# Kernel tuning notes

Measured on AMD Instinct MI355X. Metric: run time of the kernel, lower is better.

The kernel has to match this reference:

```python
import jax, jax.numpy as jnp
import numpy as np
import math

N_HEADS = 8
LN_EPS = 1e-5

def _layernorm(x, g, b):
    m = jnp.mean(x, axis=-1, keepdims=True)
    v = jnp.var(x, axis=-1, keepdims=True)
    return (x - m) / jnp.sqrt(v + LN_EPS) * g + b

def _elu_feature(x):
    return jax.nn.elu(x) + 1.0

def _recurrence(Q, K, V, decay, reverse):
    # Q,K,V: (B,H,T,d); decay: (H,)
    B, H, T, d = Q.shape
    lamS = decay[None, :, None, None]
    lamz = decay[None, :, None]
    def step(carry, inp):
        S, z = carry
        q, k, v = inp
        S = lamS * S + k[..., :, None] * v[..., None, :]       # (B,H,d,d)
        z = lamz * z + k                                        # (B,H,d)
        y_raw = jnp.einsum('bhd,bhde->bhe', q, S)
        c_raw = jnp.sum(q * z, axis=-1)
        qk = jnp.sum(q * k, axis=-1, keepdims=True)
        return (S, z), (y_raw - 0.5 * qk * v, c_raw - 0.5 * qk[..., 0])
    S0 = jnp.zeros((B, H, d, d), Q.dtype)
    z0 = jnp.zeros((B, H, d), Q.dtype)
    qs = jnp.moveaxis(Q, 2, 0)
    ks = jnp.moveaxis(K, 2, 0)
    vs = jnp.moveaxis(V, 2, 0)
    _, (Y, C) = jax.lax.scan(step, (S0, z0), (qs, ks, vs), reverse=reverse)
    return jnp.moveaxis(Y, 0, 2), jnp.moveaxis(C, 0, 2)  # (B,H,T,d),(B,H,T)

def setup_inputs() -> dict:
    B, T, D, F = 2, 2048, 512, 2048
    key = jax.random.key(0)
    ks = jax.random.split(key, 8)
    std = 0.02
    return {
        'x': jax.random.normal(ks[0], (B, T, D), jnp.float32),
        'mask': jnp.zeros((B, T), dtype=bool),
        'Wq': jax.random.normal(ks[1], (D, D), jnp.float32) * std,
        'Wk': jax.random.normal(ks[2], (D, D), jnp.float32) * std,
        'Wv': jax.random.normal(ks[3], (D, D), jnp.float32) * std,
        'Wo': jax.random.normal(ks[4], (D, D), jnp.float32) * std,
        'bo': jnp.zeros((D,), jnp.float32),
        'g1': jnp.ones((D,), jnp.float32),
        'b1': jnp.zeros((D,), jnp.float32),
        'g2': jnp.ones((D,), jnp.float32),
        'b2': jnp.zeros((D,), jnp.float32),
        'W1': jax.random.normal(ks[5], (F, D), jnp.float32) * std,
        'bf1': jnp.zeros((F,), jnp.float32),
        'W2': jax.random.normal(ks[6], (D, F), jnp.float32) * std,
        'bf2': jnp.zeros((D,), jnp.float32),
        'decay_logit': jnp.full((N_HEADS,), math.log(9.0), jnp.float32),
    }

def reference(x, mask, Wq, Wk, Wv, Wo, bo, g1, b1, g2, b2, W1, bf1, W2, bf2, decay_logit):
    B, T, D = x.shape
    H = N_HEADS
    hd = D // H
    residual = x
    xn = _layernorm(x, g1, b1)
    def proj(W):
        return jnp.einsum('btd,od->bto', xn, W).reshape(B, T, H, hd).transpose(0, 2, 1, 3)
    Q = _elu_feature(proj(Wq))
    K = _elu_feature(proj(Wk))
    V = proj(Wv)
    pad = (~mask).astype(x.dtype)[:, None, :, None]  # (B,1,T,1)
    K = K * pad
    V = V * pad
    decay = jax.nn.sigmoid(decay_logit)
    Yf, Cf = _recurrence(Q, K, V, decay, reverse=False)
    Yb, Cb = _recurrence(Q, K, V, decay, reverse=True)
    denom = jnp.clip((Cf + Cb)[..., None], 1e-6)
    out = (Yf + Yb) / denom                       # (B,H,T,d)
    out = out.transpose(0, 2, 1, 3).reshape(B, T, D)
    out = jnp.einsum('btd,od->bto', out, Wo) + bo
    x = residual + out
    h = _layernorm(x, g2, b2)
    ffn = jnp.einsum('btd,fd->btf', h, W1) + bf1
    ffn = jax.nn.gelu(ffn, approximate=False)
    ffn = jnp.einsum('btf,df->btd', ffn, W2) + bf2
    return x + ffn
```

## Files before the change

### kernel.cpp

```cpp
#include <hip/hip_runtime.h>
#include <math.h>

#define BB 2
#define TT 2048
#define DD 512
#define FF 2048
#define HH 8
#define BT 4096
#define NC 32
#define CK 64

typedef __bf16 bf16_t;
typedef bf16_t bf16x8 __attribute__((ext_vector_type(8)));
typedef bf16_t bf16x4 __attribute__((ext_vector_type(4)));
typedef float f32x4 __attribute__((ext_vector_type(4)));

typedef const __attribute__((address_space(1))) void* gas_p;
typedef __attribute__((address_space(3))) void* las_p;

__device__ __forceinline__ void async16(const void* g, void* l) {
  __builtin_amdgcn_global_load_lds((gas_p)g, (las_p)l, 16, 0, 0);
}

#define PIPE_SYNC(vm) asm volatile("s_waitcnt lgkmcnt(0) vmcnt(" vm ")\n\ts_barrier" ::: "memory")

__global__ __launch_bounds__(256) void ln_cast_kernel(
    const float* __restrict__ x, const float* __restrict__ g, const float* __restrict__ bb,
    bf16_t* __restrict__ out,
    const float* __restrict__ Wq, const float* __restrict__ Wk,
    const float* __restrict__ Wv, const float* __restrict__ Wo,
    const float* __restrict__ W1, const float* __restrict__ W2,
    bf16_t* __restrict__ wdst) {
  int t = threadIdx.x;
  if (blockIdx.x >= BT) {
    size_t i = ((size_t)(blockIdx.x - BT) * 256 + t) * 8;
    const float* src; size_t off;
    if (i < 262144)       { src = Wq; off = i; }
    else if (i < 524288)  { src = Wk; off = i - 262144; }
    else if (i < 786432)  { src = Wv; off = i - 524288; }
    else if (i < 1048576) { src = Wo; off = i - 786432; }
    else if (i < 2097152) { src = W1; off = i - 1048576; }
    else                  { src = W2; off = i - 2097152; }
    float4 a = *(const float4*)(src + off);
    float4 b = *(const float4*)(src + off + 4);
    bf16x8 o;
    o[0] = (bf16_t)a.x; o[1] = (bf16_t)a.y; o[2] = (bf16_t)a.z; o[3] = (bf16_t)a.w;
    o[4] = (bf16_t)b.x; o[5] = (bf16_t)b.y; o[6] = (bf16_t)b.z; o[7] = (bf16_t)b.w;
    *(bf16x8*)(wdst + i) = o;
    return;
  }
  int row = blockIdx.x;
  const float* xr = x + (size_t)row * DD;
  float v0 = xr[t], v1 = xr[t + 256];
  float s = v0 + v1, sq = v0 * v0 + v1 * v1;
  for (int o = 32; o; o >>= 1) { s += __shfl_down(s, o); sq += __shfl_down(sq, o); }
  __shared__ float red[8];
  __shared__ float mv[2];
  int w = t >> 6;
  if ((t & 63) == 0) { red[w] = s; red[4 + w] = sq; }
  __syncthreads();
  if (t == 0) {
    float S = red[0] + red[1] + red[2] + red[3];
    float Q = red[4] + red[5] + red[6] + red[7];
    float m = S * (1.f / 512.f);
    float var = Q * (1.f / 512.f) - m * m;
    mv[0] = m; mv[1] = rsqrtf(var + 1e-5f);
  }
  __syncthreads();
  float m = mv[0], r = mv[1];
  out[(size_t)row * DD + t]       = (bf16_t)((v0 - m) * r * g[t] + bb[t]);
  out[(size_t)row * DD + t + 256] = (bf16_t)((v1 - m) * r * g[t + 256] + bb[t + 256]);
}

template<int MODE>
__global__ __launch_bounds__(256) void mfma_gemm(
    const bf16_t* __restrict__ A, const bf16_t* __restrict__ B, int K, int NT,
    bf16_t* __restrict__ Qo, bf16_t* __restrict__ Ko, bf16_t* __restrict__ Vo,
    bf16_t* __restrict__ Ob, const float* __restrict__ bias,
    const unsigned char* __restrict__ mask) {
  __shared__ __align__(16) bf16_t smem[3 * 8192];
  int tid = threadIdx.x;
  int bid = blockIdx.x;
  int xcd = bid & 7;
  int tmp = bid >> 3;
  int nt = tmp % NT;
  int mt = (tmp / NT) * 8 + xcd;
  int n0 = nt * 128, m0 = mt * 128;
  int elt = tid * 8;
  int srow = elt >> 5, scol = elt & 31;
  const bf16_t* Ag = A + (size_t)(m0 + srow) * K + scol;
  const bf16_t* Bg = B + (size_t)(n0 + srow) * K + scol;
  size_t hstep = (size_t)64 * K;
  int NS = K >> 5;
#define ISSUE(s) { bf16_t* st = smem + ((s) % 3) * 8192; int k0 = (s) * 32; \
    async16(Ag + k0, st + elt); async16(Ag + k0 + hstep, st + 2048 + elt); \
    async16(Bg + k0, st + 4096 + elt); async16(Bg + k0 + hstep, st + 6144 + elt); }
  ISSUE(0); ISSUE(1);
  f32x4 acc[4][4] = {};
  int w = tid >> 6, l = tid & 63;
  int wm = (w >> 1) * 64, wn = (w & 1) * 64;
  int fr = l & 15, fk = (l >> 4) * 8;
  for (int i = 0; i < NS; i++) {
    if (i < NS - 1) PIPE_SYNC("4");
    else            PIPE_SYNC("0");
    if (i + 2 < NS) ISSUE(i + 2);
    const bf16_t* As = smem + (i % 3) * 8192;
    const bf16_t* Bs = As + 4096;
    bf16x8 af[4], bfr[4];
#pragma unroll
    for (int ii = 0; ii < 4; ii++) af[ii] = *(const bf16x8*)&As[(wm + ii * 16 + fr) * 32 + fk];
#pragma unroll
    for (int j = 0; j < 4; j++) bfr[j] = *(const bf16x8*)&Bs[(wn + j * 16 + fr) * 32 + fk];
#pragma unroll
    for (int ii = 0; ii < 4; ii++)
#pragma unroll
      for (int j = 0; j < 4; j++)
        acc[ii][j] = __builtin_amdgcn_mfma_f32_16x16x32_bf16(af[ii], bfr[j], acc[ii][j], 0, 0, 0);
  }
#undef ISSUE
  __syncthreads();
  const int CST = 136;
  int cn = l & 15, cr = (l >> 4) * 4;
  bf16_t* outp;
  int ldc, ncol0;
  if (MODE == 0) {
    int seg = n0 >> 9;
    outp = seg == 0 ? Qo : (seg == 1 ? Ko : Vo);
    ldc = 512; ncol0 = n0 & 511;
  } else {
    outp = Ob; ldc = 2048; ncol0 = n0;
  }
#pragma unroll
  for (int i = 0; i < 4; i++) {
#pragma unroll
    for (int r = 0; r < 4; r++) {
      int mrow = wm + i * 16 + cr + r;
      float p = 1.f;
      if (MODE == 0) p = mask[m0 + mrow] ? 0.f : 1.f;
#pragma unroll
      for (int j = 0; j < 4; j++) {
        int ncol = wn + j * 16 + cn;
        float v = acc[i][j][r];
        float ov;
        if (MODE == 0) {
          int seg = n0 >> 9;
          float e = v > 0.f ? v + 1.f : expf(v);
          ov = seg == 0 ? e : (seg == 1 ? e * p : v * p);
        } else {
          float t2 = v + bias[ncol0 + ncol];
          ov = 0.5f * t2 * (1.f + erff(t2 * 0.70710678118654752f));
        }
        smem[mrow * CST + ncol] = (bf16_t)ov;
      }
    }
  }
  __syncthreads();
#pragma unroll
  for (int it = 0; it < 8; it++) {
    int vec = tid + it * 256;
    int row = vec >> 4;
    int col = (vec & 15) * 8;
    bf16x8 v8 = *(const bf16x8*)&smem[row * CST + col];
    *(bf16x8*)(outp + (size_t)(m0 + row) * ldc + ncol0 + col) = v8;
  }
}

template<int KPER>
__global__ __launch_bounds__(256) void mfma_gemm_pk(
    const bf16_t* __restrict__ A, const bf16_t* __restrict__ B, int Kst,
    bf16_t* __restrict__ P0, bf16_t* __restrict__ P1) {
  __shared__ __align__(16) bf16_t smem[4 * 6144];
  int tid = threadIdx.x;
  int bid = blockIdx.x;
  int xcd = bid & 7;
  int tmp = bid >> 3;
  int nt = tmp & 7;
  int mt = (tmp >> 3) * 8 + xcd;
  int n0 = nt * 64, m0 = mt * 128;
  int kb = blockIdx.y * KPER;
  bf16_t* P = blockIdx.y ? P1 : P0;
  int elt = tid * 8;
  int arow = elt >> 5, acol = elt & 31;
  const bf16_t* Ag = A + (size_t)(m0 + arow) * Kst + acol;
  const bf16_t* Bg = B + (size_t)(n0 + arow) * Kst + acol;
  size_t hstep = (size_t)64 * Kst;
  const int NS = KPER >> 5;
#define ISSUE(s) { bf16_t* st = smem + ((s) & 3) * 6144; int k0 = kb + (s) * 32; \
    async16(Ag + k0, st + elt); async16(Ag + k0 + hstep, st + 2048 + elt); \
    async16(Bg + k0, st + 4096 + elt); }
  ISSUE(0); ISSUE(1); ISSUE(2);
  f32x4 acc[4][2] = {};
  int w = tid >> 6, l = tid & 63;
  int wm = (w >> 1) * 64, wn = (w & 1) * 32;
  int fr = l & 15, fk = (l >> 4) * 8;
  for (int i = 0; i < NS; i++) {
    int rem = NS - 1 - i;
    if (rem >= 2)      PIPE_SYNC("6");
    else if (rem == 1) PIPE_SYNC("3");
    else               PIPE_SYNC("0");
    if (i + 3 < NS) ISSUE(i + 3);
    const bf16_t* As = smem + (i & 3) * 6144;
    const bf16_t* Bs = As + 4096;
    bf16x8 af[4], bfr[2];
#pragma unroll
    for (int ii = 0; ii < 4; ii++) af[ii] = *(const bf16x8*)&As[(wm + ii * 16 + fr) * 32 + fk];
#pragma unroll
    for (int j = 0; j < 2; j++) bfr[j] = *(const bf16x8*)&Bs[(wn + j * 16 + fr) * 32 + fk];
#pragma unroll
    for (int ii = 0; ii < 4; ii++)
#pragma unroll
      for (int j = 0; j < 2; j++)
        acc[ii][j] = __builtin_amdgcn_mfma_f32_16x16x32_bf16(af[ii], bfr[j], acc[ii][j], 0, 0, 0);
  }
#undef ISSUE
  __syncthreads();
  const int PST = 72;
  int cn = l & 15, cr = (l >> 4) * 4;
#pragma unroll
  for (int i = 0; i < 4; i++)
#pragma unroll
    for (int r = 0; r < 4; r++) {
      int mrow = wm + i * 16 + cr + r;
#pragma unroll
      for (int j = 0; j < 2; j++) {
        int ncol = wn + j * 16 + cn;
        smem[mrow * PST + ncol] = (bf16_t)acc[i][j][r];
      }
    }
  __syncthreads();
#pragma unroll
  for (int it = 0; it < 4; it++) {
    int vec = tid + it * 256;
    int row = vec >> 3;
    int col = (vec & 7) * 8;
    bf16x8 v8 = *(const bf16x8*)&smem[row * PST + col];
    *(bf16x8*)(P + (size_t)(m0 + row) * 512 + n0 + col) = v8;
  }
}

__global__ __launch_bounds__(256) void reduce2_kernel(
    const bf16_t* __restrict__ P0, const bf16_t* __restrict__ P1,
    const float* __restrict__ bias, const float* __restrict__ resid,
    float* __restrict__ o) {
  size_t idx = ((size_t)blockIdx.x * 256 + threadIdx.x) * 4;
  int n = (int)(idx & 511);
  bf16x4 a4 = *(const bf16x4*)(P0 + idx);
  bf16x4 b4 = *(const bf16x4*)(P1 + idx);
  float4 rr = *(const float4*)(resid + idx);
  float4 bi = *(const float4*)(bias + n);
  *(float4*)(o + idx) = make_float4(
      (float)a4[0] + (float)b4[0] + bi.x + rr.x,
      (float)a4[1] + (float)b4[1] + bi.y + rr.y,
      (float)a4[2] + (float)b4[2] + bi.z + rr.z,
      (float)a4[3] + (float)b4[3] + bi.w + rr.w);
}

__global__ __launch_bounds__(256) void reduce_ln_kernel(
    const bf16_t* __restrict__ P0, const bf16_t* __restrict__ P1,
    const float* __restrict__ bias, const float* __restrict__ resid,
    float* __restrict__ x2, const float* __restrict__ g, const float* __restrict__ bb,
    bf16_t* __restrict__ out) {
  int row = blockIdx.x;
  int t = threadIdx.x;
  size_t o0 = (size_t)row * DD + t;
  size_t o1 = o0 + 256;
  float v0 = (float)P0[o0] + (float)P1[o0] + bias[t] + resid[o0];
  float v1 = (float)P0[o1] + (float)P1[o1] + bias[t + 256] + resid[o1];
  x2[o0] = v0; x2[o1] = v1;
  float s = v0 + v1, sq = v0 * v0 + v1 * v1;
  for (int o = 32; o; o >>= 1) { s += __shfl_down(s, o); sq += __shfl_down(sq, o); }
  __shared__ float red[8];
  __shared__ float mv[2];
  int w = t >> 6;
  if ((t & 63) == 0) { red[w] = s; red[4 + w] = sq; }
  __syncthreads();
  if (t == 0) {
    float S = red[0] + red[1] + red[2] + red[3];
    float Q = red[4] + red[5] + red[6] + red[7];
    float m = S * (1.f / 512.f);
    float var = Q * (1.f / 512.f) - m * m;
    mv[0] = m; mv[1] = rsqrtf(var + 1e-5f);
  }
  __syncthreads();
  float m = mv[0], r = mv[1];
  out[o0] = (bf16_t)((v0 - m) * r * g[t] + bb[t]);
  out[o1] = (bf16_t)((v1 - m) * r * g[t + 256] + bb[t + 256]);
}

__global__ __launch_bounds__(256) void chunk_summary_kernel(
    const bf16_t* __restrict__ Kb, const bf16_t* __restrict__ Vb,
    const float* __restrict__ dl, bf16_t* __restrict__ Sst, float* __restrict__ zst) {
  int chunk = blockIdx.x, bh = blockIdx.y;
  int b = bh >> 3, h = bh & 7;
  int t0 = chunk * CK;
  int tid = threadIdx.x;
  __shared__ __align__(16) float Ks[64][64];
  __shared__ __align__(16) float Vs[64][64];
  __shared__ float pw[72];
  float lam = 1.f / (1.f + expf(-dl[h]));
  if (tid <= 64) pw[tid] = powf(lam, (float)tid);
  int lrow = tid >> 2, lq = tid & 3;
  for (int q = 0; q < 2; q++) {
    int c = lq * 16 + q * 8;
    size_t g = ((size_t)(b * TT + t0 + lrow)) * DD + (size_t)h * 64 + c;
    bf16x8 k8 = *(const bf16x8*)(Kb + g);
    bf16x8 v8 = *(const bf16x8*)(Vb + g);
#pragma unroll
    for (int u = 0; u < 8; u++) { Ks[lrow][c + u] = (float)k8[u]; Vs[lrow][c + u] = (float)v8[u]; }
  }
  __syncthreads();
  int e1 = tid & 63;
  int e2b = (tid >> 6) * 16;
  float af_[16], ab_[16];
#pragma unroll
  for (int r = 0; r < 16; r++) { af_[r] = 0.f; ab_[r] = 0.f; }
  float zf = 0.f, zb = 0.f;
  for (int j = 0; j < 64; j++) {
    float kj = Ks[j][e1];
    float kf = pw[63 - j] * kj;
    float kb2 = pw[j] * kj;
    if (tid < 64) { zf += kf; zb += kb2; }
#pragma unroll
    for (int rr = 0; rr < 16; rr += 4) {
      float4 v4 = *(const float4*)&Vs[j][e2b + rr];
      af_[rr]     += kf * v4.x;  ab_[rr]     += kb2 * v4.x;
      af_[rr + 1] += kf * v4.y;  ab_[rr + 1] += kb2 * v4.y;
      af_[rr + 2] += kf * v4.z;  ab_[rr + 2] += kb2 * v4.z;
      af_[rr + 3] += kf * v4.w;  ab_[rr + 3] += kb2 * v4.w;
    }
  }
  size_t bfr = ((size_t)bh * NC + chunk) * 4096;
  size_t bbr = (((size_t)16 + bh) * NC + chunk) * 4096;
#pragma unroll
  for (int r = 0; r < 16; r++) {
    Sst[bfr + (size_t)(e2b + r) * 64 + e1] = (bf16_t)af_[r];
    Sst[bbr + (size_t)(e2b + r) * 64 + e1] = (bf16_t)ab_[r];
  }
  if (tid < 64) {
    zst[((size_t)bh * NC + chunk) * 64 + tid] = zf;
    zst[(((size_t)16 + bh) * NC + chunk) * 64 + tid] = zb;
  }
}

__global__ __launch_bounds__(1024) void scan_kernel(bf16_t* __restrict__ Sst,
                                                    float* __restrict__ zst,
                                                    const float* __restrict__ dl) {
  int bh = blockIdx.x, dir = blockIdx.y;
  int h = bh & 7;
  int tid = threadIdx.x;
  float lam = 1.f / (1.f + expf(-dl[h]));
  float lamC = powf(lam, 64.f);
  size_t base = ((size_t)dir * 16 + bh) * (size_t)NC * 4096 + (size_t)tid * 4;
  float s0 = 0.f, s1 = 0.f, s2 = 0.f, s3 = 0.f;
  for (int g = 0; g < 4; g++) {
    bf16x4 L[8];
#pragma unroll
    for (int i = 0; i < 8; i++) {
      int s = g * 8 + i;
      int c = dir ? (NC - 1 - s) : s;
      L[i] = *(bf16x4*)(Sst + base + (size_t)c * 4096);
    }
#pragma unroll
    for (int i = 0; i < 8; i++) {
      int s = g * 8 + i;
      int c = dir ? (NC - 1 - s) : s;
      s0 = s0 * lamC + (float)L[i][0];
      s1 = s1 * lamC + (float)L[i][1];
      s2 = s2 * lamC + (float)L[i][2];
      s3 = s3 * lamC + (float)L[i][3];
      bf16x4 o;
      o[0] = (bf16_t)s0; o[1] = (bf16_t)s1; o[2] = (bf16_t)s2; o[3] = (bf16_t)s3;
      *(bf16x4*)(Sst + base + (size_t)c * 4096) = o;
    }
  }
  if (tid < 64) {
    size_t zb = ((size_t)dir * 16 + bh) * (size_t)NC * 64 + tid;
    float z = 0.f;
    for (int g = 0; g < 4; g++) {
      float zL[8];
#pragma unroll
      for (int i = 0; i < 8; i++) {
        int s = g * 8 + i;
        int c = dir ? (NC - 1 - s) : s;
        zL[i] = zst[zb + (size_t)c * 64];
      }
#pragma unroll
      for (int i = 0; i < 8; i++) {
        int s = g * 8 + i;
        int c = dir ? (NC - 1 - s) : s;
        z = z * lamC + zL[i];
        zst[zb + (size_t)c * 64] = z;
      }
    }
  }
}

#define AST 72
__global__ __launch_bounds__(256) void chunk_attn_kernel(
    const bf16_t* __restrict__ Qb, const bf16_t* __restrict__ Kb, const bf16_t* __restrict__ Vb,
    const bf16_t* __restrict__ Sst, const float* __restrict__ zst, const float* __restrict__ dl,
    bf16_t* __restrict__ attnb) {
  int chunk = blockIdx.x, bh = blockIdx.y;
  int b = bh >> 3, h = bh & 7;
  int t0 = chunk * CK;
  int tid = threadIdx.x;
  __shared__ __align__(16) bf16_t Qa[64 * AST];
  __shared__ __align__(16) bf16_t KA[64 * AST];
  __shared__ __align__(16) bf16_t Vt[64 * AST];
  __shared__ __align__(16) bf16_t Sft[64 * AST];
  __shared__ __align__(16) bf16_t Sbt[64 * AST];
  __shared__ float rowpart[64][16];
  __shared__ float zpf[64], zpb[64];
  __shared__ float den[64];
  __shared__ float pw[72];
  float lam = 1.f / (1.f + expf(-dl[h]));
  if (tid <= 64) pw[tid] = powf(lam, (float)tid);
  int lrow = tid >> 2, lq = tid & 3;
  for (int q = 0; q < 2; q++) {
    int c = lq * 16 + q * 8;
    size_t g = ((size_t)(b * TT + t0 + lrow)) * DD + (size_t)h * 64 + c;
    bf16x8 q8 = *(const bf16x8*)(Qb + g);
    bf16x8 k8 = *(const bf16x8*)(Kb + g);
    bf16x8 v8 = *(const bf16x8*)(Vb + g);
    *(bf16x8*)&Qa[lrow * AST + c] = q8;
    *(bf16x8*)&KA[lrow * AST + c] = k8;
#pragma unroll
    for (int u = 0; u < 8; u++) Vt[(c + u) * AST + lrow] = v8[u];
  }
  {
    int c16 = lq * 16;
    if (chunk > 0) {
      const bf16_t* src = Sst + ((size_t)bh * NC + chunk - 1) * 4096 + (size_t)lrow * 64 + c16;
      *(bf16x8*)&Sft[lrow * AST + c16] = *(const bf16x8*)src;
      *(bf16x8*)&Sft[lrow * AST + c16 + 8] = *(const bf16x8*)(src + 8);
      if (tid < 64) zpf[tid] = zst[((size_t)bh * NC + chunk - 1) * 64 + tid];
    } else {
      bf16x8 z8 = {};
      *(bf16x8*)&Sft[lrow * AST + c16] = z8;
      *(bf16x8*)&Sft[lrow * AST + c16 + 8] = z8;
      if (tid < 64) zpf[tid] = 0.f;
    }
    if (chunk < NC - 1) {
      const bf16_t* src = Sst + (((size_t)16 + bh) * NC + chunk + 1) * 4096 + (size_t)lrow * 64 + c16;
      *(bf16x8*)&Sbt[lrow * AST + c16] = *(const bf16x8*)src;
      *(bf16x8*)&Sbt[lrow * AST + c16 + 8] = *(const bf16x8*)(src + 8);
      if (tid < 64) zpb[tid] = zst[(((size_t)16 + bh) * NC + chunk + 1) * 64 + tid];
    } else {
      bf16x8 z8 = {};
      *(bf16x8*)&Sbt[lrow * AST + c16] = z8;
      *(bf16x8*)&Sbt[lrow * AST + c16 + 8] = z8;
      if (tid < 64) zpb[tid] = 0.f;
    }
  }
  __syncthreads();
  int w = tid >> 6, l = tid & 63;
  int fr = l & 15, fk = (l >> 4) * 8;
  int cr = (l >> 4) * 4, cn = l & 15;
  int ms = w * 16;
  bf16x8 qf0 = *(const bf16x8*)&Qa[(ms + fr) * AST + fk];
  bf16x8 qf1 = *(const bf16x8*)&Qa[(ms + fr) * AST + 32 + fk];
  f32x4 aqk[4] = {};
#pragma unroll
  for (int t = 0; t < 4; t++) {
    bf16x8 kf0 = *(const bf16x8*)&KA[(t * 16 + fr) * AST + fk];
    bf16x8 kf1 = *(const bf16x8*)&KA[(t * 16 + fr) * AST + 32 + fk];
    aqk[t] = __builtin_amdgcn_mfma_f32_16x16x32_bf16(qf0, kf0, aqk[t], 0, 0, 0);
    aqk[t] = __builtin_amdgcn_mfma_f32_16x16x32_bf16(qf1, kf1, aqk[t], 0, 0, 0);
  }
  __syncthreads();
  float rs[4] = {0.f, 0.f, 0.f, 0.f};
#pragma unroll
  for (int t = 0; t < 4; t++) {
#pragma unroll
    for (int r = 0; r < 4; r++) {
      int i = ms + cr + r;
      int j = t * 16 + cn;
      int dd = i > j ? i - j : j - i;
      float v = aqk[t][r] * pw[dd];
      rs[r] += v;
      KA[i * AST + j] = (bf16_t)v;
    }
  }
#pragma unroll
  for (int r = 0; r < 4; r++) rowpart[ms + cr + r][cn] = rs[r];
  __syncthreads();
  bf16x8 af0 = *(const bf16x8*)&KA[(ms + fr) * AST + fk];
  bf16x8 af1 = *(const bf16x8*)&KA[(ms + fr) * AST + 32 + fk];
  f32x4 aY[4] = {}, aSf[4] = {}, aSb[4] = {};
#pragma unroll
  for (int t = 0; t < 4; t++) {
    bf16x8 vf0 = *(const bf16x8*)&Vt[(t * 16 + fr) * AST + fk];
    bf16x8 vf1 = *(const bf16x8*)&Vt[(t * 16 + fr) * AST + 32 + fk];
    aY[t] = __builtin_amdgcn_mfma_f32_16x16x32_bf16(af0, vf0, aY[t], 0, 0, 0);
    aY[t] = __builtin_amdgcn_mfma_f32_16x16x32_bf16(af1, vf1, aY[t], 0, 0, 0);
    bf16x8 sf0 = *(const bf16x8*)&Sft[(t * 16 + fr) * AST + fk];
    bf16x8 sf1 = *(const bf16x8*)&Sft[(t * 16 + fr) * AST + 32 + fk];
    aSf[t] = __builtin_amdgcn_mfma_f32_16x16x32_bf16(qf0, sf0, aSf[t], 0, 0, 0);
    aSf[t] = __builtin_amdgcn_mfma_f32_16x16x32_bf16(qf1, sf1, aSf[t], 0, 0, 0);
    bf16x8 sb0 = *(const bf16x8*)&Sbt[(t * 16 + fr) * AST + fk];
    bf16x8 sb1 = *(const bf16x8*)&Sbt[(t * 16 + fr) * AST + 32 + fk];
    aSb[t] = __builtin_amdgcn_mfma_f32_16x16x32_bf16(qf0, sb0, aSb[t], 0, 0, 0);
    aSb[t] = __builtin_amdgcn_mfma_f32_16x16x32_bf16(qf1, sb1, aSb[t], 0, 0, 0);
  }
  if (tid < 64) {
    int i = tid;
    float s = 0.f;
#pragma unroll
    for (int xx = 0; xx < 16; xx++) s += rowpart[i][xx];
    float czf = 0.f, czb = 0.f;
    for (int c = 0; c < 64; c += 8) {
      bf16x8 q8 = *(const bf16x8*)&Qa[i * AST + c];
#pragma unroll
      for (int u = 0; u < 8; u++) { czf += (float)q8[u] * zpf[c + u]; czb += (float)q8[u] * zpb[c + u]; }
    }
    den[i] = s + pw[i + 1] * czf + pw[64 - i] * czb;
  }
  __syncthreads();
#pragma unroll
  for (int t = 0; t < 4; t++) {
#pragma unroll
    for (int r = 0; r < 4; r++) {
      int i = ms + cr + r;
      int e = t * 16 + cn;
      float lrf = pw[i + 1], lrb = pw[64 - i];
      float inv = 1.f / fmaxf(den[i], 1e-6f);
      float val = (aY[t][r] + lrf * aSf[t][r] + lrb * aSb[t][r]) * inv;
      attnb[((size_t)(b * TT + t0 + i)) * DD + (size_t)h * 64 + e] = (bf16_t)val;
    }
  }
}

extern "C" void kernel_launch(void* const* d_in, const int* in_sizes, int n_in,
                              void* d_out, int out_size, void* d_ws, size_t ws_size,
                              hipStream_t stream) {
  const float* x   = (const float*)d_in[0];
  const unsigned char* mask = (const unsigned char*)d_in[1];
  const float* Wq  = (const float*)d_in[2];
  const float* Wk  = (const float*)d_in[3];
  const float* Wv  = (const float*)d_in[4];
  const float* Wo  = (const float*)d_in[5];
  const float* bo  = (const float*)d_in[6];
  const float* g1  = (const float*)d_in[7];
  const float* b1  = (const float*)d_in[8];
  const float* g2  = (const float*)d_in[9];
  const float* b2  = (const float*)d_in[10];
  const float* W1  = (const float*)d_in[11];
  const float* bf1 = (const float*)d_in[12];
  const float* W2  = (const float*)d_in[13];
  const float* bf2 = (const float*)d_in[14];
  const float* dl  = (const float*)d_in[15];
  float* out = (float*)d_out;

  float* ws = (float*)d_ws;
  const size_t U = (size_t)BT * DD;
  float* Qr  = ws;
  float* Kr  = ws + U;
  float* Vr  = ws + 2 * U;
  float* R3  = ws + 3 * U;
  float* R4  = ws + 4 * U;
  float* x2  = ws + 5 * U;
  bf16_t* Sstb = (bf16_t*)(ws + 6 * U);
  float* zst = ws + 8 * U;
  bf16_t* wall = (bf16_t*)(ws + 8 * U + 131072);
  bf16_t* Qb    = (bf16_t*)Qr;
  bf16_t* Kb    = (bf16_t*)Kr;
  bf16_t* Vb    = (bf16_t*)Vr;
  bf16_t* xnb   = (bf16_t*)R3;
  bf16_t* attnb = (bf16_t*)x2;
  bf16_t* h2b   = (bf16_t*)Qr;
  bf16_t* ffn1b = (bf16_t*)Kr;
  bf16_t* Wob = wall + 786432;
  bf16_t* W1b = wall + 1048576;
  bf16_t* W2b = wall + 2097152;
  bf16_t* Ps0 = (bf16_t*)R3;
  bf16_t* Ps1 = (bf16_t*)R4;

  ln_cast_kernel<<<BT + 1536, 256, 0, stream>>>(x, g1, b1, xnb, Wq, Wk, Wv, Wo, W1, W2, wall);
  mfma_gemm<0><<<384, 256, 0, stream>>>(xnb, wall, 512, 12, Qb, Kb, Vb,
                                        nullptr, nullptr, mask);
  chunk_summary_kernel<<<dim3(NC, 16), 256, 0, stream>>>(Kb, Vb, dl, Sstb, zst);
  scan_kernel<<<dim3(16, 2), 1024, 0, stream>>>(Sstb, zst, dl);
  chunk_attn_kernel<<<dim3(NC, 16), 256, 0, stream>>>(Qb, Kb, Vb, Sstb, zst, dl, attnb);
  mfma_gemm_pk<256><<<dim3(256, 2), 256, 0, stream>>>(attnb, Wob, 512, Ps0, Ps1);
  reduce_ln_kernel<<<BT, 256, 0, stream>>>(Ps0, Ps1, bo, x, x2, g2, b2, h2b);
  mfma_gemm<2><<<512, 256, 0, stream>>>(h2b, W1b, 512, 16, nullptr, nullptr, nullptr,
                                        ffn1b, bf1, nullptr);
  mfma_gemm_pk<1024><<<dim3(256, 2), 256, 0, stream>>>(ffn1b, W2b, 2048, Ps0, Ps1);
  reduce2_kernel<<<2048, 256, 0, stream>>>(Ps0, Ps1, bf2, x2, out);
}
```

Before: 196.9 us.

## Replace split-K GEMMs with fused-epilogue 64-wide GEMM and widen scan grid

Replaces the split-K partial GEMMs and their separate reduce kernels with a single gemm64 kernel. Its epilogue adds bias and residual in fp32 directly, and LayerNorm moves into a standalone ln2 kernel. The QKV projection also uses this 128x64 tile GEMM with 768 blocks instead of the earlier 384-block path. The scan kernel is split across 16 sub-blocks per head and direction with scalar elements, which raises parallelism. Together these remove the bf16 partial-sum round trips and two reduction kernels, at the cost of fewer blocks (256) in the Wo and W2 GEMMs and more, smaller blocks in the scan.

```diff
diff --git a/kernel.cpp b/kernel.cpp
--- a/kernel.cpp
+++ b/kernel.cpp
@@ -51,6 +51,33 @@
   }
   int row = blockIdx.x;
   const float* xr = x + (size_t)row * DD;
+  float v0 = xr[t], v1 = xr[t + 256];
+  float s = v0 + v1, sq = v0 * v0 + v1 * v1;
+  for (int o = 32; o; o >>= 1) { s += __shfl_down(s, o); sq += __shfl_down(sq, o); }
+  __shared__ float red[8];
+  __shared__ float mv[2];
+  int w = t >> 6;
+  if ((t & 63) == 0) { red[w] = s; red[4 + w] = sq; }
+  __syncthreads();
+  if (t == 0) {
+    float S = red[0] + red[1] + red[2] + red[3];
+    float Q = red[4] + red[5] + red[6] + red[7];
+    float m = S * (1.f / 512.f);
+    float var = Q * (1.f / 512.f) - m * m;
+    mv[0] = m; mv[1] = rsqrtf(var + 1e-5f);
+  }
+  __syncthreads();
+  float m = mv[0], r = mv[1];
+  out[(size_t)row * DD + t]       = (bf16_t)((v0 - m) * r * g[t] + bb[t]);
+  out[(size_t)row * DD + t + 256] = (bf16_t)((v1 - m) * r * g[t + 256] + bb[t + 256]);
+}
+
+__global__ __launch_bounds__(256) void ln2_kernel(
+    const float* __restrict__ x2, const float* __restrict__ g, const float* __restrict__ bb,
+    bf16_t* __restrict__ out) {
+  int row = blockIdx.x;
+  int t = threadIdx.x;
+  const float* xr = x2 + (size_t)row * DD;
   float v0 = xr[t], v1 = xr[t + 256];
   float s = v0 + v1, sq = v0 * v0 + v1 * v1;
   for (int o = 32; o; o >>= 1) { s += __shfl_down(s, o); sq += __shfl_down(sq, o); }
@@ -165,27 +192,27 @@
   }
 }
 
-template<int KPER>
-__global__ __launch_bounds__(256) void mfma_gemm_pk(
-    const bf16_t* __restrict__ A, const bf16_t* __restrict__ B, int Kst,
-    bf16_t* __restrict__ P0, bf16_t* __restrict__ P1) {
+template<int MODE>
+__global__ __launch_bounds__(256) void gemm64(
+    const bf16_t* __restrict__ A, const bf16_t* __restrict__ B, int K, int NT,
+    bf16_t* __restrict__ Qo, bf16_t* __restrict__ Ko, bf16_t* __restrict__ Vo,
+    const float* __restrict__ bias, const float* __restrict__ resid,
+    float* __restrict__ fout, const unsigned char* __restrict__ mask) {
   __shared__ __align__(16) bf16_t smem[4 * 6144];
   int tid = threadIdx.x;
   int bid = blockIdx.x;
   int xcd = bid & 7;
   int tmp = bid >> 3;
-  int nt = tmp & 7;
-  int mt = (tmp >> 3) * 8 + xcd;
+  int nt = tmp % NT;
+  int mt = (tmp / NT) * 8 + xcd;
   int n0 = nt * 64, m0 = mt * 128;
-  int kb = blockIdx.y * KPER;
-  bf16_t* P = blockIdx.y ? P1 : P0;
   int elt = tid * 8;
-  int arow = elt >> 5, acol = elt & 31;
-  const bf16_t* Ag = A + (size_t)(m0 + arow) * Kst + acol;
-  const bf16_t* Bg = B + (size_t)(n0 + arow) * Kst + acol;
-  size_t hstep = (size_t)64 * Kst;
-  const int NS = KPER >> 5;
-#define ISSUE(s) { bf16_t* st = smem + ((s) & 3) * 6144; int k0 = kb + (s) * 32; \
+  int srow = elt >> 5, scol = elt & 31;
+  const bf16_t* Ag = A + (size_t)(m0 + srow) * K + scol;
+  const bf16_t* Bg = B + (size_t)(n0 + srow) * K + scol;
+  size_t hstep = (size_t)64 * K;
+  const int NS = K >> 5;
+#define ISSUE(s) { bf16_t* st = smem + ((s) & 3) * 6144; int k0 = (s) * 32; \
     async16(Ag + k0, st + elt); async16(Ag + k0 + hstep, st + 2048 + elt); \
     async16(Bg + k0, st + 4096 + elt); }
   ISSUE(0); ISSUE(1); ISSUE(2);
@@ -214,77 +241,65 @@
   }
 #undef ISSUE
   __syncthreads();
-  const int PST = 72;
   int cn = l & 15, cr = (l >> 4) * 4;
-#pragma unroll
-  for (int i = 0; i < 4; i++)
-#pragma unroll
-    for (int r = 0; r < 4; r++) {
-      int mrow = wm + i * 16 + cr + r;
-#pragma unroll
-      for (int j = 0; j < 2; j++) {
-        int ncol = wn + j * 16 + cn;
-        smem[mrow * PST + ncol] = (bf16_t)acc[i][j][r];
+  if (MODE == 0) {
+    const int CST = 72;
+    int seg = n0 >> 9;
+#pragma unroll
+    for (int i = 0; i < 4; i++) {
+#pragma unroll
+      for (int r = 0; r < 4; r++) {
+        int mrow = wm + i * 16 + cr + r;
+        float p = mask[m0 + mrow] ? 0.f : 1.f;
+#pragma unroll
+        for (int j = 0; j < 2; j++) {
+          int ncol = wn + j * 16 + cn;
+          float v = acc[i][j][r];
+          float e = v > 0.f ? v + 1.f : expf(v);
+          float ov = seg == 0 ? e : (seg == 1 ? e * p : v * p);
+          smem[mrow * CST + ncol] = (bf16_t)ov;
+        }
       }
     }
-  __syncthreads();
-#pragma unroll
-  for (int it = 0; it < 4; it++) {
-    int vec = tid + it * 256;
-    int row = vec >> 3;
-    int col = (vec & 7) * 8;
-    bf16x8 v8 = *(const bf16x8*)&smem[row * PST + col];
-    *(bf16x8*)(P + (size_t)(m0 + row) * 512 + n0 + col) = v8;
-  }
-}
-
-__global__ __launch_bounds__(256) void reduce2_kernel(
-    const bf16_t* __restrict__ P0, const bf16_t* __restrict__ P1,
-    const float* __restrict__ bias, const float* __restrict__ resid,
-    float* __restrict__ o) {
-  size_t idx = ((size_t)blockIdx.x * 256 + threadIdx.x) * 4;
-  int n = (int)(idx & 511);
-  bf16x4 a4 = *(const bf16x4*)(P0 + idx);
-  bf16x4 b4 = *(const bf16x4*)(P1 + idx);
-  float4 rr = *(const float4*)(resid + idx);
-  float4 bi = *(const float4*)(bias + n);
-  *(float4*)(o + idx) = make_float4(
-      (float)a4[0] + (float)b4[0] + bi.x + rr.x,
-      (float)a4[1] + (float)b4[1] + bi.y + rr.y,
-      (float)a4[2] + (float)b4[2] + bi.z + rr.z,
-      (float)a4[3] + (float)b4[3] + bi.w + rr.w);
-}
-
-__global__ __launch_bounds__(256) void reduce_ln_kernel(
-    const bf16_t* __restrict__ P0, const bf16_t* __restrict__ P1,
-    const float* __restrict__ bias, const float* __restrict__ resid,
-    float* __restrict__ x2, const float* __restrict__ g, const float* __restrict__ bb,
-    bf16_t* __restrict__ out) {
-  int row = blockIdx.x;
-  int t = threadIdx.x;
-  size_t o0 = (size_t)row * DD + t;
-  size_t o1 = o0 + 256;
-  float v0 = (float)P0[o0] + (float)P1[o0] + bias[t] + resid[o0];
-  float v1 = (float)P0[o1] + (float)P1[o1] + bias[t + 256] + resid[o1];
-  x2[o0] = v0; x2[o1] = v1;
-  float s = v0 + v1, sq = v0 * v0 + v1 * v1;
-  for (int o = 32; o; o >>= 1) { s += __shfl_down(s, o); sq += __shfl_down(sq, o); }
-  __shared__ float red[8];
-  __shared__ float mv[2];
-  int w = t >> 6;
-  if ((t & 63) == 0) { red[w] = s; red[4 + w] = sq; }
-  __syncthreads();
-  if (t == 0) {
-    float S = red[0] + red[1] + red[2] + red[3];
-    float Q = red[4] + red[5] + red[6] + red[7];
-    float m = S * (1.f / 512.f);
-    float var = Q * (1.f / 512.f) - m * m;
-    mv[0] = m; mv[1] = rsqrtf(var + 1e-5f);
-  }
-  __syncthreads();
-  float m = mv[0], r = mv[1];
-  out[o0] = (bf16_t)((v0 - m) * r * g[t] + bb[t]);
-  out[o1] = (bf16_t)((v1 - m) * r * g[t + 256] + bb[t + 256]);
+    __syncthreads();
+    bf16_t* outp = seg == 0 ? Qo : (seg == 1 ? Ko : Vo);
+    int ncol0 = n0 & 511;
+#pragma unroll
+    for (int it = 0; it < 4; it++) {
+      int vec = tid + it * 256;
+      int row = vec >> 3;
+      int col = (vec & 7) * 8;
+      bf16x8 v8 = *(const bf16x8*)&smem[row * CST + col];
+      *(bf16x8*)(outp + (size_t)(m0 + row) * 512 + ncol0 + col) = v8;
+    }
+  } else {
+    const int FST = 72;
+    float* smf = (float*)smem;
+#pragma unroll
+    for (int i = 0; i < 4; i++)
+#pragma unroll
+      for (int r = 0; r < 4; r++) {
+        int mrow = wm + i * 16 + cr + r;
+#pragma unroll
+        for (int j = 0; j < 2; j++) {
+          int ncol = wn + j * 16 + cn;
+          smf[mrow * FST + ncol] = acc[i][j][r];
+        }
+      }
+    __syncthreads();
+#pragma unroll
+    for (int it = 0; it < 8; it++) {
+      int vec = tid + it * 256;
+      int row = vec >> 4;
+      int col = (vec & 15) * 4;
+      size_t gidx = (size_t)(m0 + row) * 512 + n0 + col;
+      float4 v = *(const float4*)&smf[row * FST + col];
+      float4 bi = *(const float4*)(bias + n0 + col);
+      float4 rr = *(const float4*)(resid + gidx);
+      *(float4*)(fout + gidx) = make_float4(v.x + bi.x + rr.x, v.y + bi.y + rr.y,
+                                            v.z + bi.z + rr.z, v.w + bi.w + rr.w);
+    }
+  }
 }
 
 __global__ __launch_bounds__(256) void chunk_summary_kernel(
@@ -342,52 +357,50 @@
   }
 }
 
-__global__ __launch_bounds__(1024) void scan_kernel(bf16_t* __restrict__ Sst,
-                                                    float* __restrict__ zst,
-                                                    const float* __restrict__ dl) {
-  int bh = blockIdx.x, dir = blockIdx.y;
+__global__ __launch_bounds__(256) void scan_kernel(bf16_t* __restrict__ Sst,
+                                                   float* __restrict__ zst,
+                                                   const float* __restrict__ dl) {
+  int sub = blockIdx.x;
+  int bh  = blockIdx.y;
+  int dir = blockIdx.z;
   int h = bh & 7;
   int tid = threadIdx.x;
   float lam = 1.f / (1.f + expf(-dl[h]));
   float lamC = powf(lam, 64.f);
-  size_t base = ((size_t)dir * 16 + bh) * (size_t)NC * 4096 + (size_t)tid * 4;
-  float s0 = 0.f, s1 = 0.f, s2 = 0.f, s3 = 0.f;
+  int elem = sub * 256 + tid;
+  size_t base = ((size_t)dir * 16 + bh) * (size_t)NC * 4096 + elem;
+  float s = 0.f;
   for (int g = 0; g < 4; g++) {
-    bf16x4 L[8];
+    bf16_t L[8];
 #pragma unroll
     for (int i = 0; i < 8; i++) {
-      int s = g * 8 + i;
-      int c = dir ? (NC - 1 - s) : s;
-      L[i] = *(bf16x4*)(Sst + base + (size_t)c * 4096);
+      int st = g * 8 + i;
+      int c = dir ? (NC - 1 - st) : st;
+      L[i] = Sst[base + (size_t)c * 4096];
     }
 #pragma unroll
     for (int i = 0; i < 8; i++) {
-      int s = g * 8 + i;
-      int c = dir ? (NC - 1 - s) : s;
-      s0 = s0 * lamC + (float)L[i][0];
-      s1 = s1 * lamC + (float)L[i][1];
-      s2 = s2 * lamC + (float)L[i][2];
-      s3 = s3 * lamC + (float)L[i][3];
-      bf16x4 o;
-      o[0] = (bf16_t)s0; o[1] = (bf16_t)s1; o[2] = (bf16_t)s2; o[3] = (bf16_t)s3;
-      *(bf16x4*)(Sst + base + (size_t)c * 4096) = o;
-    }
-  }
-  if (tid < 64) {
+      int st = g * 8 + i;
+      int c = dir ? (NC - 1 - st) : st;
+      s = s * lamC + (float)L[i];
+      Sst[base + (size_t)c * 4096] = (bf16_t)s;
+    }
+  }
+  if (sub == 0 && tid < 64) {
     size_t zb = ((size_t)dir * 16 + bh) * (size_t)NC * 64 + tid;
     float z = 0.f;
     for (int g = 0; g < 4; g++) {
       float zL[8];
 #pragma unroll
       for (int i = 0; i < 8; i++) {
-        int s = g * 8 + i;
-        int c = dir ? (NC - 1 - s) : s;
+        int st = g * 8 + i;
+        int c = dir ? (NC - 1 - st) : st;
         zL[i] = zst[zb + (size_t)c * 64];
       }
 #pragma unroll
       for (int i = 0; i < 8; i++) {
-        int s = g * 8 + i;
-        int c = dir ? (NC - 1 - s) : s;
+        int st = g * 8 + i;
+        int c = dir ? (NC - 1 - st) : st;
         z = z * lamC + zL[i];
         zst[zb + (size_t)c * 64] = z;
       }
@@ -566,25 +579,24 @@
   bf16_t* Kb    = (bf16_t*)Kr;
   bf16_t* Vb    = (bf16_t*)Vr;
   bf16_t* xnb   = (bf16_t*)R3;
-  bf16_t* attnb = (bf16_t*)x2;
+  bf16_t* attnb = (bf16_t*)R4;
   bf16_t* h2b   = (bf16_t*)Qr;
   bf16_t* ffn1b = (bf16_t*)Kr;
   bf16_t* Wob = wall + 786432;
   bf16_t* W1b = wall + 1048576;
   bf16_t* W2b = wall + 2097152;
-  bf16_t* Ps0 = (bf16_t*)R3;
-  bf16_t* Ps1 = (bf16_t*)R4;
 
   ln_cast_kernel<<<BT + 1536, 256, 0, stream>>>(x, g1, b1, xnb, Wq, Wk, Wv, Wo, W1, W2, wall);
-  mfma_gemm<0><<<384, 256, 0, stream>>>(xnb, wall, 512, 12, Qb, Kb, Vb,
-                                        nullptr, nullptr, mask);
+  gemm64<0><<<768, 256, 0, stream>>>(xnb, wall, 512, 24, Qb, Kb, Vb,
+                                     nullptr, nullptr, nullptr, mask);
   chunk_summary_kernel<<<dim3(NC, 16), 256, 0, stream>>>(Kb, Vb, dl, Sstb, zst);
-  scan_kernel<<<dim3(16, 2), 1024, 0, stream>>>(Sstb, zst, dl);
+  scan_kernel<<<dim3(16, 16, 2), 256, 0, stream>>>(Sstb, zst, dl);
   chunk_attn_kernel<<<dim3(NC, 16), 256, 0, stream>>>(Qb, Kb, Vb, Sstb, zst, dl, attnb);
-  mfma_gemm_pk<256><<<dim3(256, 2), 256, 0, stream>>>(attnb, Wob, 512, Ps0, Ps1);
-  reduce_ln_kernel<<<BT, 256, 0, stream>>>(Ps0, Ps1, bo, x, x2, g2, b2, h2b);
+  gemm64<1><<<256, 256, 0, stream>>>(attnb, Wob, 512, 8, nullptr, nullptr, nullptr,
+                                     bo, x, x2, nullptr);
+  ln2_kernel<<<BT, 256, 0, stream>>>(x2, g2, b2, h2b);
   mfma_gemm<2><<<512, 256, 0, stream>>>(h2b, W1b, 512, 16, nullptr, nullptr, nullptr,
                                         ffn1b, bf1, nullptr);
-  mfma_gemm_pk<1024><<<dim3(256, 2), 256, 0, stream>>>(ffn1b, W2b, 2048, Ps0, Ps1);
-  reduce2_kernel<<<2048, 256, 0, stream>>>(Ps0, Ps1, bf2, x2, out);
-}
+  gemm64<1><<<256, 256, 0, stream>>>(ffn1b, W2b, 2048, 8, nullptr, nullptr, nullptr,
+                                     bf2, x2, out, nullptr);
+}
```

New measurement: 192.7 us. -2.1%, faster.
